# Optimization experiments

Measured on AMD Instinct MI355X. Metric: run time of the kernel, lower is better.

The kernel has to match this reference:

```python
import jax, jax.numpy as jnp
import numpy as np

T, B, I, H = 1024, 64, 512, 512


def setup_inputs() -> dict:
    key = jax.random.key(0)
    ks = jax.random.split(key, 7)
    s = 1.0 / np.sqrt(H).astype(np.float32)
    return {
        "x": jax.random.normal(ks[0], (T, B, I), dtype=jnp.float32),
        "h0": jax.random.normal(ks[1], (B, H), dtype=jnp.float32),
        "c0": jax.random.normal(ks[2], (B, H), dtype=jnp.float32),
        "W_ih": jax.random.normal(ks[3], (4 * H, I), dtype=jnp.float32) * s,
        "W_hh": jax.random.normal(ks[4], (4 * H, H), dtype=jnp.float32) * s,
        "b_ih": jax.random.normal(ks[5], (4 * H,), dtype=jnp.float32) * s,
        "b_hh": jax.random.normal(ks[6], (4 * H,), dtype=jnp.float32) * s,
        "alpha": jnp.ones((1,), dtype=jnp.float32),
    }


def reference(x, h0, c0, W_ih, W_hh, b_ih, b_hh, alpha):
    # Precompute input-to-hidden projections for all timesteps in one GEMM.
    # x: [T, B, I] -> xg: [T, B, 4H]
    xg = jnp.einsum("tbi,gi->tbg", x, W_ih) + b_ih
    a = alpha[0]

    def step(carry, xg_t):
        h, c = carry  # [B, H] each
        gates = xg_t + h @ W_hh.T + b_hh  # [B, 4H]
        i, f, g, o = jnp.split(gates, 4, axis=-1)
        i = jax.nn.sigmoid(i)
        f = jax.nn.sigmoid(f)
        g = jnp.tanh(g)
        o = jax.nn.sigmoid(o)
        c_new = f * c + i * g
        h_new = o * jnp.tanh(c_new)
        # alpha step-size interpolation (alpha=1 -> plain LSTM)
        c_out = a * c_new + (1.0 - a) * c
        h_out = a * h_new + (1.0 - a) * h
        return (h_out, c_out), h_out

    (hT, cT), ys = jax.lax.scan(step, (h0, c0), xg)
    return ys, hT, cT
```

## Files before the change

### kernel.cpp

```cpp
#include <hip/hip_runtime.h>

typedef __attribute__((ext_vector_type(8))) short short8;
typedef __attribute__((ext_vector_type(4))) float f32x4;
typedef __attribute__((ext_vector_type(4))) float float4v;
typedef __attribute__((ext_vector_type(4))) unsigned short u16x4;
typedef __attribute__((ext_vector_type(4))) unsigned int u32x4;

#define T_TOT   1024
#define BATCH   64
#define HID     512
#define G4      2048
#define NGRID   128
#define BH      (BATCH * HID)

static __device__ __forceinline__ unsigned short f2bf(float x) {
  union { float f; unsigned u; } v; v.f = x;
  unsigned r = v.u + 0x7FFFu + ((v.u >> 16) & 1u);
  return (unsigned short)(r >> 16);
}
static __device__ __forceinline__ float sigm(float x) {
  return 1.0f / (1.0f + __expf(-x));
}
static __device__ __forceinline__ float tanh_fast(float x) {
  return 1.0f - 2.0f / (__expf(2.0f * x) + 1.0f);
}
static __device__ __forceinline__ void bar_lds() {
  asm volatile("s_waitcnt lgkmcnt(0)" ::: "memory");
  __builtin_amdgcn_s_barrier();
  asm volatile("" ::: "memory");
}

__global__ void init_k(const float* __restrict__ h0, const float* __restrict__ c0,
                       unsigned int* __restrict__ hb2, float* __restrict__ cst,
                       float* __restrict__ hst) {
  const int i = blockIdx.x * 256 + threadIdx.x;
  if (i < BH) {
    const float h = h0[i];
    hb2[i] = (unsigned)f2bf(h);
    hb2[BH + i] = 0xFFFF0000u;
    hst[i] = h;
    cst[i] = c0[i];
  }
}

static __device__ __forceinline__ void gemm_body(
    int bm, int bn, const float* __restrict__ A, const float* __restrict__ W,
    const float* __restrict__ bih, const float* __restrict__ bhh,
    float* __restrict__ xzp) {
  __shared__ unsigned short As[128 * 64];
  __shared__ unsigned short Bs[128 * 64];
  const int tid  = threadIdx.x;
  const int lane = tid & 63;
  const int wid  = tid >> 6;
  const int wm   = (wid >> 1) * 64;
  const int wn   = (wid & 1) * 64;
  const int l15  = lane & 15;
  const int l4   = lane >> 4;

  f32x4 acc[4][4];
#pragma unroll
  for (int mt = 0; mt < 4; ++mt)
#pragma unroll
    for (int nt = 0; nt < 4; ++nt) acc[mt][nt] = f32x4{0.f, 0.f, 0.f, 0.f};

  const float* Ab = A + (long)bm * 128 * 512;
  const float* Wb = W + (long)bn * 128 * 512;
  const int r0 = tid >> 4;
  const int cq = (tid & 15) * 4;

  for (int k0 = 0; k0 < 512; k0 += 64) {
#pragma unroll
    for (int pass = 0; pass < 8; ++pass) {
      const int r = pass * 16 + r0;
      const float4v va = *(const float4v*)(Ab + (long)r * 512 + k0 + cq);
      const float4v vb = *(const float4v*)(Wb + (long)r * 512 + k0 + cq);
      u16x4 pa, pb;
#pragma unroll
      for (int j = 0; j < 4; ++j) { pa[j] = f2bf(va[j]); pb[j] = f2bf(vb[j]); }
      const int boff = r * 128 + ((cq * 2) ^ ((r & 7) << 4));
      *(u16x4*)((char*)As + boff) = pa;
      *(u16x4*)((char*)Bs + boff) = pb;
    }
    __syncthreads();
#pragma unroll
    for (int kk = 0; kk < 2; ++kk) {
      short8 af[4], bfv[4];
#pragma unroll
      for (int mt = 0; mt < 4; ++mt) {
        const int row = wm + mt * 16 + l15;
        af[mt] = *(const short8*)((const char*)As + row * 128 +
                                  ((kk * 64 + l4 * 16) ^ ((row & 7) << 4)));
      }
#pragma unroll
      for (int nt = 0; nt < 4; ++nt) {
        const int row = wn + nt * 16 + l15;
        bfv[nt] = *(const short8*)((const char*)Bs + row * 128 +
                                   ((kk * 64 + l4 * 16) ^ ((row & 7) << 4)));
      }
#pragma unroll
      for (int mt = 0; mt < 4; ++mt)
#pragma unroll
        for (int nt = 0; nt < 4; ++nt)
          acc[mt][nt] = __builtin_amdgcn_mfma_f32_16x16x32_bf16(af[mt], bfv[nt], acc[mt][nt], 0, 0, 0);
    }
    __syncthreads();
  }

#pragma unroll
  for (int nt = 0; nt < 4; ++nt) {
    const int gn = bn * 128 + wn + nt * 16 + l15;
    const float bias = bih[gn] + bhh[gn];
    const int g2   = gn >> 9;
    const int hh   = gn & 511;
    const int nb2  = hh >> 5;
    const int col2 = hh & 31;
#pragma unroll
    for (int mt = 0; mt < 4; ++mt) {
      const int m0 = bm * 128 + wm + mt * 16 + l4 * 4;
#pragma unroll
      for (int r = 0; r < 4; ++r) {
        const int m = m0 + r;
        const int tt2 = m >> 6, brow = m & 63;
        const int mb2 = brow >> 3, r2 = brow & 7;
        xzp[((((size_t)tt2 * 8 + mb2) * 16 + nb2) << 10) + r2 * 128 + g2 * 32 + col2] =
            acc[mt][nt][r] + bias;
      }
    }
  }
}

__global__ __launch_bounds__(256) void xz_gemm(
    const float* __restrict__ A, const float* __restrict__ W,
    const float* __restrict__ bih, const float* __restrict__ bhh,
    float* __restrict__ xzp) {
  gemm_body(blockIdx.x, blockIdx.y, A, W, bih, bhh, xzp);
}

__global__ __launch_bounds__(256, 1) void fused_chunk(
    const float* __restrict__ xnext,
    const float* __restrict__ Wih,
    const float* __restrict__ bih, const float* __restrict__ bhh,
    float* __restrict__ xzp_next,
    const float* __restrict__ xzp_cur,
    const float* __restrict__ Whh,
    const float* __restrict__ alpha_p,
    float* __restrict__ out,
    unsigned int* __restrict__ hb2,
    float* __restrict__ cst, float* __restrict__ hst,
    int t0, int Tc) {
  const int bx = blockIdx.x;
  if (bx >= NGRID) {
    const int g = bx - NGRID;
    gemm_body(g >> 4, g & 15, xnext, Wih, bih, bhh, xzp_next);
    return;
  }

  const int mb  = bx & 7;
  const int nb  = bx >> 3;
  const int rb0 = mb * 8;
  const int hs0 = nb * 32;
  const int tid = threadIdx.x;
  const int lane = tid & 63;
  const int w   = tid >> 6;
  const int l15 = lane & 15;
  const int l4  = lane >> 4;

  __shared__ __align__(16) unsigned short h_lds[16 * HID];
  __shared__ __align__(16) float gates[4][16][36];

  short8 wf0[16], wf1[16];
  {
    const float* wr0 = Whh + (long)(w * HID + hs0 + l15) * HID + l4 * 8;
    const float* wr1 = Whh + (long)(w * HID + hs0 + 16 + l15) * HID + l4 * 8;
#pragma unroll
    for (int ks = 0; ks < 16; ++ks) {
      float4v lo = *(const float4v*)(wr0 + ks * 32);
      float4v hi = *(const float4v*)(wr0 + ks * 32 + 4);
      short8 f;
#pragma unroll
      for (int j = 0; j < 4; ++j) { f[j] = (short)f2bf(lo[j]); f[j+4] = (short)f2bf(hi[j]); }
      wf0[ks] = f;
      lo = *(const float4v*)(wr1 + ks * 32);
      hi = *(const float4v*)(wr1 + ks * 32 + 4);
#pragma unroll
      for (int j = 0; j < 4; ++j) { f[j] = (short)f2bf(lo[j]); f[j+4] = (short)f2bf(hi[j]); }
      wf1[ks] = f;
    }
  }
  const float a = alpha_p[0];
  const float oma = 1.0f - a;

  for (int idx = tid; idx < 512; idx += 256) {
    const int r = 8 + (idx >> 6), c = idx & 63;
    *(u32x4*)((char*)h_lds + c * 256 + ((r ^ (c & 15)) << 4)) = u32x4{0u,0u,0u,0u};
  }

  const int em = tid >> 5;
  const int en = tid & 31;
  float cp = cst[(long)(rb0 + em) * HID + hs0 + en];
  float hp = hst[(long)(rb0 + em) * HID + hs0 + en];
  bar_lds();

  const long YS = (long)T_TOT * BATCH * HID;
  const int swr = tid >> 5;
  const int swc = (tid & 31) * 16;

  float xzv[8];
  u32x4 sv[4];
  {
    const float* xb = xzp_cur + ((((size_t)0 * 8 + mb) * 16 + nb) << 10);
#pragma unroll
    for (int n = 0; n < 2; ++n)
#pragma unroll
      for (int j = 0; j < 4; ++j) {
        const float* p = xb + ((l4 * 4 + j) & 7) * 128 + w * 32 + n * 16 + l15;
        asm volatile("global_load_dword %0, %1, off" : "=v"(xzv[n*4+j]) : "v"(p));
      }
    const unsigned int* p0 = hb2 + (size_t)(t0 & 1) * BH +
                             (size_t)(rb0 + swr) * HID + swc;
#pragma unroll
    for (int i = 0; i < 4; ++i)
      asm volatile("global_load_dwordx4 %0, %1, off sc0" : "=v"(sv[i]) : "v"(p0 + i * 4));
  }

  for (int tt = 0; tt < Tc; ++tt) {
    const int t = t0 + tt;

    if (tt == 0) asm volatile("s_waitcnt vmcnt(0)" ::: "memory");
    else         asm volatile("s_waitcnt vmcnt(1)" ::: "memory");
    __builtin_amdgcn_sched_barrier(0);

    {
      const unsigned wantHi = ((unsigned)t) << 16;
      const unsigned int* p0 = hb2 + (size_t)(t & 1) * BH +
                               (size_t)(rb0 + swr) * HID + swc;
      for (;;) {
        unsigned bad = 0u;
#pragma unroll
        for (int i = 0; i < 4; ++i) {
          unsigned d = 0u;
#pragma unroll
          for (int j = 0; j < 4; ++j) d |= (sv[i][j] ^ wantHi);
          if (d & 0xFFFF0000u) bad |= (1u << i);
        }
        if (!__any(bad != 0u)) break;
#pragma unroll
        for (int i = 0; i < 4; ++i)
          if (bad & (1u << i))
            asm volatile("global_load_dwordx4 %0, %1, off sc0 sc1"
                         : "=v"(sv[i]) : "v"(p0 + i * 4));
        asm volatile("s_waitcnt vmcnt(0)" ::: "memory");
        __builtin_amdgcn_sched_barrier(0);
      }
    }

#pragma unroll
    for (int q = 0; q < 2; ++q) {
      u32x4 pk;
      pk[0] = __builtin_amdgcn_perm(sv[q*2][1],   sv[q*2][0],   0x05040100u);
      pk[1] = __builtin_amdgcn_perm(sv[q*2][3],   sv[q*2][2],   0x05040100u);
      pk[2] = __builtin_amdgcn_perm(sv[q*2+1][1], sv[q*2+1][0], 0x05040100u);
      pk[3] = __builtin_amdgcn_perm(sv[q*2+1][3], sv[q*2+1][2], 0x05040100u);
      const int c = (tid & 31) * 2 + q;
      *(u32x4*)((char*)h_lds + c * 256 + ((swr ^ (c & 15)) << 4)) = pk;
    }
    bar_lds();

    f32x4 ac00, ac01, ac10, ac11;
    ac00 = f32x4{xzv[0], xzv[1], xzv[2], xzv[3]};
    ac10 = f32x4{xzv[4], xzv[5], xzv[6], xzv[7]};
    ac01 = f32x4{0.f, 0.f, 0.f, 0.f};
    ac11 = ac01;
#pragma unroll
    for (int ks = 0; ks < 16; ks += 2) {
      const int c0 = ks * 4 + l4;
      const int c1 = c0 + 4;
      const short8 af0 = *(const short8*)((const char*)h_lds + c0 * 256 +
                                          ((l15 ^ (c0 & 15)) << 4));
      const short8 af1 = *(const short8*)((const char*)h_lds + c1 * 256 +
                                          ((l15 ^ (c1 & 15)) << 4));
      ac00 = __builtin_amdgcn_mfma_f32_16x16x32_bf16(af0, wf0[ks],   ac00, 0, 0, 0);
      ac10 = __builtin_amdgcn_mfma_f32_16x16x32_bf16(af0, wf1[ks],   ac10, 0, 0, 0);
      ac01 = __builtin_amdgcn_mfma_f32_16x16x32_bf16(af1, wf0[ks+1], ac01, 0, 0, 0);
      ac11 = __builtin_amdgcn_mfma_f32_16x16x32_bf16(af1, wf1[ks+1], ac11, 0, 0, 0);
    }
    {
      const f32x4 s0 = ac00 + ac01;
      const f32x4 s1 = ac10 + ac11;
#pragma unroll
      for (int r = 0; r < 4; ++r) {
        gates[w][l4 * 4 + r][l15]      = s0[r];
        gates[w][l4 * 4 + r][16 + l15] = s1[r];
      }
    }
    bar_lds();

    const float gi = gates[0][em][en], gf = gates[1][em][en];
    const float gg = gates[2][em][en], go = gates[3][em][en];
    const float ii = sigm(gi), ff = sigm(gf), oo = sigm(go);
    const float g  = tanh_fast(gg);
    const float cn = ff * cp + ii * g;
    const float hn = oo * tanh_fast(cn);
    const float co = a * cn + oma * cp;
    const float ho = a * hn + oma * hp;
    cp = co;
    hp = ho;

    {
      unsigned int* dst = hb2 + (size_t)((t + 1) & 1) * BH +
                          (long)(rb0 + em) * HID + hs0 + en;
      const unsigned w32 = (((unsigned)(t + 1)) << 16) | (unsigned)f2bf(ho);
      asm volatile("global_store_dword %0, %1, off sc0 sc1"
                   :: "v"((const void*)dst), "v"(w32) : "memory");
      asm volatile("global_store_dword %0, %1, off"
                   :: "v"((const void*)dst), "v"(w32) : "memory");
    }

    if (tt < Tc - 1) {
      const float* xb = xzp_cur + ((((size_t)(tt + 1) * 8 + mb) * 16 + nb) << 10);
#pragma unroll
      for (int n = 0; n < 2; ++n)
#pragma unroll
        for (int j = 0; j < 4; ++j) {
          const float* p = xb + ((l4 * 4 + j) & 7) * 128 + w * 32 + n * 16 + l15;
          asm volatile("global_load_dword %0, %1, off" : "=v"(xzv[n*4+j]) : "v"(p));
        }
      const unsigned int* pn = hb2 + (size_t)((t + 1) & 1) * BH +
                               (size_t)(rb0 + swr) * HID + swc;
#pragma unroll
      for (int i = 0; i < 4; ++i)
        asm volatile("global_load_dwordx4 %0, %1, off sc0" : "=v"(sv[i]) : "v"(pn + i * 4));
      const float* op = out + ((long)t * BATCH + rb0 + em) * HID + hs0 + en;
      asm volatile("global_store_dword %0, %1, off"
                   :: "v"((const void*)op), "v"(ho) : "memory");
    }
  }

  {
    const int tl = t0 + Tc - 1;
    out[((long)tl * BATCH + rb0 + em) * HID + hs0 + en] = hp;
    if (t0 + Tc == T_TOT) {
      out[YS + (long)(rb0 + em) * HID + hs0 + en] = hp;
      out[YS + BATCH * HID + (long)(rb0 + em) * HID + hs0 + en] = cp;
    }
    cst[(long)(rb0 + em) * HID + hs0 + en] = cp;
    hst[(long)(rb0 + em) * HID + hs0 + en] = hp;
  }
}

extern "C" void kernel_launch(void* const* d_in, const int* in_sizes, int n_in,
                              void* d_out, int out_size, void* d_ws, size_t ws_size,
                              hipStream_t stream) {
  const float* x     = (const float*)d_in[0];
  const float* h0    = (const float*)d_in[1];
  const float* c0    = (const float*)d_in[2];
  const float* W_ih  = (const float*)d_in[3];
  const float* W_hh  = (const float*)d_in[4];
  const float* b_ih  = (const float*)d_in[5];
  const float* b_hh  = (const float*)d_in[6];
  const float* alpha = (const float*)d_in[7];
  float* out = (float*)d_out;

  int Tc = 128;
  while ((size_t)2 * (size_t)Tc * 524288ull + 786432ull > ws_size && Tc > 2) Tc >>= 1;

  char* ws = (char*)d_ws;
  unsigned int* hb2 = (unsigned int*)(ws + 0);
  float* cst = (float*)(ws + 262144);
  float* hst = (float*)(ws + 393216);
  float* xzp0 = (float*)(ws + 786432);
  float* xzp1 = (float*)(ws + 786432 + (size_t)Tc * 524288ull);
  float* xzp[2] = {xzp0, xzp1};

  const int nchunk = T_TOT / Tc;
  const size_t xoff = (size_t)Tc * BATCH * 512;
  const int nG = (Tc / 2) * 16;

  init_k<<<128, 256, 0, stream>>>(h0, c0, hb2, cst, hst);
  {
    dim3 gg(Tc / 2, 16);
    xz_gemm<<<gg, 256, 0, stream>>>(x, W_ih, b_ih, b_hh, xzp[0]);
  }
  for (int k = 0; k < nchunk; ++k) {
    const bool last = (k == nchunk - 1);
    const int grid = NGRID + (last ? 0 : nG);
    fused_chunk<<<grid, 256, 0, stream>>>(
        x + (size_t)(k + 1) * xoff, W_ih, b_ih, b_hh, xzp[(k + 1) & 1],
        xzp[k & 1], W_hh, alpha, out, hb2, cst, hst, k * Tc, Tc);
  }
}
```

Baseline: 2.444 ms.

## Write own hidden slice to LDS locally and relax cross-block polling loads

Each lane now writes its own freshly computed bf16 hidden value directly into the LDS operand tile, and the lanes owning that slice skip global polling for it on later steps. Retry polling loads use the lighter cache policy for the first few attempts before falling back to the system-coherent variant. The x-projection prefetch is moved earlier, right after the gate barrier, and the waitcnt is adjusted so the h loads can stay in flight. This aims to shorten the per-timestep global synchronisation latency, at the cost of extra control flow and possible stale reads if the cache policy is not coherent enough.

```diff
diff --git a/kernel.cpp b/kernel.cpp
--- a/kernel.cpp
+++ b/kernel.cpp
@@ -204,6 +204,9 @@
   const long YS = (long)T_TOT * BATCH * HID;
   const int swr = tid >> 5;
   const int swc = (tid & 31) * 16;
+  const bool ownlane = ((en >> 1) == nb);
+  const int c3 = nb * 4 + (en >> 3);
+  char* ownp = (char*)h_lds + c3 * 256 + ((em ^ (c3 & 15)) << 4) + (en & 7) * 2;
 
   float xzv[8];
   u32x4 sv[4];
@@ -227,42 +230,56 @@
     const int t = t0 + tt;
 
     if (tt == 0) asm volatile("s_waitcnt vmcnt(0)" ::: "memory");
-    else         asm volatile("s_waitcnt vmcnt(1)" ::: "memory");
+    else         asm volatile("s_waitcnt vmcnt(3)" ::: "memory");
     __builtin_amdgcn_sched_barrier(0);
 
     {
       const unsigned wantHi = ((unsigned)t) << 16;
+      const bool own = (tt > 0) && ownlane;
       const unsigned int* p0 = hb2 + (size_t)(t & 1) * BH +
                                (size_t)(rb0 + swr) * HID + swc;
+      int tries = 0;
       for (;;) {
         unsigned bad = 0u;
-#pragma unroll
-        for (int i = 0; i < 4; ++i) {
-          unsigned d = 0u;
-#pragma unroll
-          for (int j = 0; j < 4; ++j) d |= (sv[i][j] ^ wantHi);
-          if (d & 0xFFFF0000u) bad |= (1u << i);
+        if (!own) {
+#pragma unroll
+          for (int i = 0; i < 4; ++i) {
+            unsigned d = (sv[i][0] ^ wantHi) | (sv[i][1] ^ wantHi) |
+                         (sv[i][2] ^ wantHi) | (sv[i][3] ^ wantHi);
+            if (d & 0xFFFF0000u) bad |= (1u << i);
+          }
         }
         if (!__any(bad != 0u)) break;
-#pragma unroll
-        for (int i = 0; i < 4; ++i)
-          if (bad & (1u << i))
-            asm volatile("global_load_dwordx4 %0, %1, off sc0 sc1"
-                         : "=v"(sv[i]) : "v"(p0 + i * 4));
+        if (tries < 3) {
+#pragma unroll
+          for (int i = 0; i < 4; ++i)
+            if (bad & (1u << i))
+              asm volatile("global_load_dwordx4 %0, %1, off sc0"
+                           : "=v"(sv[i]) : "v"(p0 + i * 4));
+        } else {
+#pragma unroll
+          for (int i = 0; i < 4; ++i)
+            if (bad & (1u << i))
+              asm volatile("global_load_dwordx4 %0, %1, off sc0 sc1"
+                           : "=v"(sv[i]) : "v"(p0 + i * 4));
+        }
+        ++tries;
         asm volatile("s_waitcnt vmcnt(0)" ::: "memory");
         __builtin_amdgcn_sched_barrier(0);
       }
-    }
-
-#pragma unroll
-    for (int q = 0; q < 2; ++q) {
-      u32x4 pk;
-      pk[0] = __builtin_amdgcn_perm(sv[q*2][1],   sv[q*2][0],   0x05040100u);
-      pk[1] = __builtin_amdgcn_perm(sv[q*2][3],   sv[q*2][2],   0x05040100u);
-      pk[2] = __builtin_amdgcn_perm(sv[q*2+1][1], sv[q*2+1][0], 0x05040100u);
-      pk[3] = __builtin_amdgcn_perm(sv[q*2+1][3], sv[q*2+1][2], 0x05040100u);
-      const int c = (tid & 31) * 2 + q;
-      *(u32x4*)((char*)h_lds + c * 256 + ((swr ^ (c & 15)) << 4)) = pk;
+
+      if (!own) {
+#pragma unroll
+        for (int q = 0; q < 2; ++q) {
+          u32x4 pk;
+          pk[0] = __builtin_amdgcn_perm(sv[q*2][1],   sv[q*2][0],   0x05040100u);
+          pk[1] = __builtin_amdgcn_perm(sv[q*2][3],   sv[q*2][2],   0x05040100u);
+          pk[2] = __builtin_amdgcn_perm(sv[q*2+1][1], sv[q*2+1][0], 0x05040100u);
+          pk[3] = __builtin_amdgcn_perm(sv[q*2+1][3], sv[q*2+1][2], 0x05040100u);
+          const int c = en * 2 + q;
+          *(u32x4*)((char*)h_lds + c * 256 + ((swr ^ (c & 15)) << 4)) = pk;
+        }
+      }
     }
     bar_lds();
 
@@ -295,6 +312,17 @@
     }
     bar_lds();
 
+    if (tt < Tc - 1) {
+      const float* xb = xzp_cur + ((((size_t)(tt + 1) * 8 + mb) * 16 + nb) << 10);
+#pragma unroll
+      for (int n = 0; n < 2; ++n)
+#pragma unroll
+        for (int j = 0; j < 4; ++j) {
+          const float* p = xb + ((l4 * 4 + j) & 7) * 128 + w * 32 + n * 16 + l15;
+          asm volatile("global_load_dword %0, %1, off" : "=v"(xzv[n*4+j]) : "v"(p));
+        }
+    }
+
     const float gi = gates[0][em][en], gf = gates[1][em][en];
     const float gg = gates[2][em][en], go = gates[3][em][en];
     const float ii = sigm(gi), ff = sigm(gf), oo = sigm(go);
@@ -305,31 +333,28 @@
     const float ho = a * hn + oma * hp;
     cp = co;
     hp = ho;
+    const unsigned hob = (unsigned)f2bf(ho);
+
+    *(unsigned short*)ownp = (unsigned short)hob;
+
+    if (tt < Tc - 1) {
+      const unsigned int* pn = hb2 + (size_t)((t + 1) & 1) * BH +
+                               (size_t)(rb0 + swr) * HID + swc;
+#pragma unroll
+      for (int i = 0; i < 4; ++i)
+        asm volatile("global_load_dwordx4 %0, %1, off sc0" : "=v"(sv[i]) : "v"(pn + i * 4));
+    }
 
     {
       unsigned int* dst = hb2 + (size_t)((t + 1) & 1) * BH +
                           (long)(rb0 + em) * HID + hs0 + en;
-      const unsigned w32 = (((unsigned)(t + 1)) << 16) | (unsigned)f2bf(ho);
+      const unsigned w32 = (((unsigned)(t + 1)) << 16) | hob;
       asm volatile("global_store_dword %0, %1, off sc0 sc1"
                    :: "v"((const void*)dst), "v"(w32) : "memory");
       asm volatile("global_store_dword %0, %1, off"
                    :: "v"((const void*)dst), "v"(w32) : "memory");
     }
-
     if (tt < Tc - 1) {
-      const float* xb = xzp_cur + ((((size_t)(tt + 1) * 8 + mb) * 16 + nb) << 10);
-#pragma unroll
-      for (int n = 0; n < 2; ++n)
-#pragma unroll
-        for (int j = 0; j < 4; ++j) {
-          const float* p = xb + ((l4 * 4 + j) & 7) * 128 + w * 32 + n * 16 + l15;
-          asm volatile("global_load_dword %0, %1, off" : "=v"(xzv[n*4+j]) : "v"(p));
-        }
-      const unsigned int* pn = hb2 + (size_t)((t + 1) & 1) * BH +
-                               (size_t)(rb0 + swr) * HID + swc;
-#pragma unroll
-      for (int i = 0; i < 4; ++i)
-        asm volatile("global_load_dwordx4 %0, %1, off sc0" : "=v"(sv[i]) : "v"(pn + i * 4));
       const float* op = out + ((long)t * BATCH + rb0 + em) * HID + hs0 + en;
       asm volatile("global_store_dword %0, %1, off"
                    :: "v"((const void*)op), "v"(ho) : "memory");
```

After: 3.967 ms. +62.3%, slower.
